# Kernel tuning notes

Hardware: AMD Instinct MI355X
Metric: run time of the kernel (lower is better)

The kernel has to match this reference:

```python
import jax, jax.numpy as jnp
import numpy as np

B, S, D = 2, 2048, 4096
H, KVH, HD = 32, 8, 128
N_REP = H // KVH
ROPE_THETA = 10000.0


def setup_inputs() -> dict:
    key = jax.random.key(0)
    ks = jax.random.split(key, 6)
    x_norm = jax.random.normal(ks[0], (B, S, D), dtype=jnp.float32)
    scale = 0.02
    wq = jax.random.normal(ks[1], (H * HD, D), dtype=jnp.float32) * scale
    wk = jax.random.normal(ks[2], (KVH * HD, D), dtype=jnp.float32) * scale
    wv = jax.random.normal(ks[3], (KVH * HD, D), dtype=jnp.float32) * scale
    wo = jax.random.normal(ks[4], (D, H * HD), dtype=jnp.float32) * scale
    # RoPE tables: freqs_cis[t, j] = exp(i * t * theta^{-2j/HD})
    inv_freq = 1.0 / (ROPE_THETA ** (jnp.arange(0, HD, 2, dtype=jnp.float32) / HD))  # [HD/2]
    angles = jnp.arange(S, dtype=jnp.float32)[:, None] * inv_freq[None, :]  # [S, HD/2]
    freqs_cos = jnp.cos(angles)
    freqs_sin = jnp.sin(angles)
    # causal additive mask (0 on/below diagonal, -1e9 above)
    mask = jnp.where(jnp.arange(S)[None, :] > jnp.arange(S)[:, None], jnp.float32(-1e9), jnp.float32(0.0))
    return {"x_norm": x_norm, "wq": wq, "wk": wk, "wv": wv, "wo": wo,
            "freqs_cos": freqs_cos, "freqs_sin": freqs_sin, "mask": mask, "start_pos": 0}


def _apply_rope(t, cos, sin):
    # t: [B, S, h, HD]; cos/sin: [S, HD/2] -> rotate consecutive pairs
    tr = t.reshape(*t.shape[:-1], HD // 2, 2)
    t0, t1 = tr[..., 0], tr[..., 1]
    c = cos[None, :, None, :]
    s = sin[None, :, None, :]
    out = jnp.stack([t0 * c - t1 * s, t0 * s + t1 * c], axis=-1)
    return out.reshape(t.shape)


def reference(x_norm, wq, wk, wv, wo, freqs_cos, freqs_sin, mask, start_pos):
    # QKV projections (torch Linear: y = x @ W.T)
    xq = jnp.einsum("bsd,ed->bse", x_norm, wq).reshape(B, S, H, HD)
    xk = jnp.einsum("bsd,ed->bse", x_norm, wk).reshape(B, S, KVH, HD)
    xv = jnp.einsum("bsd,ed->bse", x_norm, wv).reshape(B, S, KVH, HD)
    xq = _apply_rope(xq, freqs_cos, freqs_sin)
    xk = _apply_rope(xk, freqs_cos, freqs_sin)
    # start_pos == 0 prefill: cache slice [:start_pos+seqlen] == freshly written xk/xv
    keys = jnp.repeat(xk, N_REP, axis=2)    # [B, S, H, HD] (GQA repeat_kv)
    values = jnp.repeat(xv, N_REP, axis=2)  # [B, S, H, HD]
    scale = 1.0 / np.sqrt(HD).astype(np.float32)
    scores = jnp.einsum("bqhd,bkhd->bhqk", xq, keys) * scale
    scores = scores + mask[None, None, :, :]
    probs = jax.nn.softmax(scores.astype(jnp.float32), axis=-1).astype(xq.dtype)
    out = jnp.einsum("bhqk,bkhd->bqhd", probs, values).reshape(B, S, H * HD)
    return jnp.einsum("bse,de->bsd", out, wo)
```

## Files before the change

kernel.cpp:

```cpp
#include <hip/hip_runtime.h>
#include <stdint.h>

#define B_N 2
#define S_N 2048
#define D_N 4096
#define H_N 32
#define KVH_N 8
#define HD_N 128
#define NQT (S_N / 64)
#define QK_SCALE 0.08838834764831845f

typedef __attribute__((ext_vector_type(8))) short bf16x8;
typedef __attribute__((ext_vector_type(4))) float f32x4;

__device__ __forceinline__ unsigned short f2bf(float f) {
    union { float f; unsigned u; } v; v.f = f;
    unsigned u = v.u;
    u += 0x7fffu + ((u >> 16) & 1u);
    return (unsigned short)(u >> 16);
}
__device__ __forceinline__ float bf2f(unsigned short h) {
    union { unsigned u; float f; } v; v.u = ((unsigned)h) << 16;
    return v.f;
}

__device__ __forceinline__ void gl16(const unsigned short* g, unsigned short* l) {
    __builtin_amdgcn_global_load_lds(
        (const __attribute__((address_space(1))) void*)g,
        (__attribute__((address_space(3))) void*)l, 16, 0, 0);
}

__global__ void __launch_bounds__(256) conv_f32_bf16(const float* __restrict__ in,
                                                     unsigned short* __restrict__ out) {
    int i = (blockIdx.x * 256 + threadIdx.x) * 4;
    float4 v = *(const float4*)(in + i);
    ushort4 o;
    o.x = f2bf(v.x); o.y = f2bf(v.y); o.z = f2bf(v.z); o.w = f2bf(v.w);
    *(ushort4*)(out + i) = o;
}

template<int HEADS, int STRIDE>
__global__ void __launch_bounds__(256) rope_kernel(unsigned short* __restrict__ t,
                                                   const float* __restrict__ cosb,
                                                   const float* __restrict__ sinb,
                                                   float scale) {
    int p = blockIdx.x * 256 + threadIdx.x;
    int i = p & 63;
    int hr = p >> 6;
    int m = hr / HEADS;
    int hh = hr - m * HEADS;
    int s = m & (S_N - 1);
    size_t off = (size_t)m * STRIDE + hh * HD_N + 2 * i;
    unsigned v = *(const unsigned*)(t + off);
    float t0 = bf2f((unsigned short)(v & 0xffffu));
    float t1 = bf2f((unsigned short)(v >> 16));
    float c = cosb[s * 64 + i], sn = sinb[s * 64 + i];
    float o0 = (t0 * c - t1 * sn) * scale;
    float o1 = (t0 * sn + t1 * c) * scale;
    *(unsigned*)(t + off) = (unsigned)f2bf(o0) | ((unsigned)f2bf(o1) << 16);
}


#define BAR() __builtin_amdgcn_s_barrier()
#define VMC4() asm volatile("s_waitcnt vmcnt(4)" ::: "memory")

template<int F32OUT>
__global__ void __launch_bounds__(512, 2)
gemm256(const unsigned short* __restrict__ A, const unsigned short* __restrict__ Bm,
        void* __restrict__ Cv, int M, int N, int K) {
    __shared__ unsigned short ldsA[2][16384];
    __shared__ unsigned short ldsB[2][16384];

    const int tid = threadIdx.x;
    const int lane = tid & 63;
    const int w = tid >> 6;
    const int li = lane & 15, lg = lane >> 4;
    const int wr = w >> 2, wc = w & 3;

    const int nwg = gridDim.x;
    const int cpx = nwg >> 3;
    const int wg = (blockIdx.x & 7) * cpx + (blockIdx.x >> 3);
    const int nbn = N >> 8;
    const int bm = wg / nbn, bn = wg - bm * nbn;
    const int m0 = bm << 8, n0 = bn << 8;

    const int rbase = ((tid >> 7) << 4) + ((tid >> 2) & 15);
    const int cstg = ((tid >> 6) & 1) * 32 + (((tid & 3) * 8) ^ (((tid >> 5) & 1) << 4));
    const unsigned short* Asrc[4];
    const unsigned short* Bsrc[4];
#pragma unroll
    for (int hj = 0; hj < 4; ++hj) {
        Asrc[hj] = A + (size_t)(m0 + hj * 64 + rbase) * K + cstg;
        Bsrc[hj] = Bm + (size_t)(n0 + hj * 64 + rbase) * K + cstg;
    }
    const int dstoff = tid * 8;
    const int kmask = K - 1;

    f32x4 acc[8][4];
#pragma unroll
    for (int i = 0; i < 8; ++i)
#pragma unroll
        for (int j = 0; j < 4; ++j) acc[i][j] = (f32x4){0.f, 0.f, 0.f, 0.f};

    const int colpart = (lg * 16) ^ ((li >> 3) << 5);

#define STG(SRC, LDSBUF, H, T) do {                                         \
        int kk_ = ((T) * 64) & kmask;                                       \
        gl16(SRC[(H)*2 + 0] + kk_, &LDSBUF[((H)*2 + 0) * 4096 + dstoff]);   \
        gl16(SRC[(H)*2 + 1] + kk_, &LDSBUF[((H)*2 + 1) * 4096 + dstoff]);   \
    } while (0)

#define LDB(buf) do {                                                        \
        _Pragma("unroll")                                                    \
        for (int ni_ = 0; ni_ < 4; ++ni_) {                                  \
            _Pragma("unroll")                                                \
            for (int ks_ = 0; ks_ < 2; ++ks_)                                \
                bfr[ni_][ks_] = *(const bf16x8*)((const char*)&ldsB[buf][0]  \
                    + (wc * 4 + ni_) * 2048 + ks_ * 1024 + li * 64 + colpart); \
        }                                                                    \
    } while (0)

#define LDA(buf, q) do {                                                     \
        _Pragma("unroll")                                                    \
        for (int m_ = 0; m_ < 2; ++m_) {                                     \
            _Pragma("unroll")                                                \
            for (int ks_ = 0; ks_ < 2; ++ks_)                                \
                af[m_][ks_] = *(const bf16x8*)((const char*)&ldsA[buf][0]    \
                    + (wr * 8 + (q) * 2 + m_) * 2048 + ks_ * 1024 + li * 64 + colpart); \
        }                                                                    \
    } while (0)

#define MFMAQ(q) do {                                                        \
        __builtin_amdgcn_s_setprio(1);                                       \
        _Pragma("unroll")                                                    \
        for (int ks_ = 0; ks_ < 2; ++ks_) {                                  \
            _Pragma("unroll")                                                \
            for (int m_ = 0; m_ < 2; ++m_) {                                 \
                _Pragma("unroll")                                            \
                for (int ni_ = 0; ni_ < 4; ++ni_)                            \
                    acc[(q)*2 + m_][ni_] = __builtin_amdgcn_mfma_f32_16x16x32_bf16( \
                        af[m_][ks_], bfr[ni_][ks_], acc[(q)*2 + m_][ni_], 0, 0, 0); \
            }                                                                \
        }                                                                    \
        __builtin_amdgcn_s_setprio(0);                                       \
    } while (0)

    STG(Asrc, ldsA[0], 0, 0); STG(Asrc, ldsA[0], 1, 0);
    STG(Bsrc, ldsB[0], 0, 0); STG(Bsrc, ldsB[0], 1, 0);
    STG(Bsrc, ldsB[1], 0, 1); STG(Bsrc, ldsB[1], 1, 1);
    VMC4();
    BAR();

    const int NIT = K >> 7;
    bf16x8 bfr[4][2], af[2][2];
#pragma unroll 1
    for (int i = 0; i < NIT; ++i) {
        const int T = 2 * i;
        LDB(0); LDA(0, 0);
        STG(Asrc, ldsA[1], 0, T + 1);
        BAR(); MFMAQ(0); BAR();
        LDA(0, 1);
        STG(Asrc, ldsA[1], 1, T + 1);
        STG(Bsrc, ldsB[0], 0, T + 2);
        BAR(); MFMAQ(1); BAR();
        LDA(0, 2);
        STG(Bsrc, ldsB[0], 1, T + 2);
        BAR(); MFMAQ(2); BAR();
        LDA(0, 3);
        BAR(); MFMAQ(3); VMC4(); BAR();
        LDB(1); LDA(1, 0);
        STG(Asrc, ldsA[0], 0, T + 2);
        BAR(); MFMAQ(0); BAR();
        LDA(1, 1);
        STG(Asrc, ldsA[0], 1, T + 2);
        BAR(); MFMAQ(1); BAR();
        LDA(1, 2);
        STG(Bsrc, ldsB[1], 0, T + 3);
        BAR(); MFMAQ(2); BAR();
        LDA(1, 3);
        STG(Bsrc, ldsB[1], 1, T + 3);
        BAR(); MFMAQ(3); VMC4(); BAR();
    }

    const int r0 = m0 + wr * 128 + lg * 4;
    const int c0 = n0 + wc * 64 + li;
    if (F32OUT) {
        float* C = (float*)Cv;
#pragma unroll
        for (int mi = 0; mi < 8; ++mi)
#pragma unroll
            for (int ni = 0; ni < 4; ++ni)
#pragma unroll
                for (int rr = 0; rr < 4; ++rr)
                    C[(size_t)(r0 + mi * 16 + rr) * N + c0 + ni * 16] = acc[mi][ni][rr];
    } else {
        unsigned short* C = (unsigned short*)Cv;
#pragma unroll
        for (int mi = 0; mi < 8; ++mi)
#pragma unroll
            for (int ni = 0; ni < 4; ++ni)
#pragma unroll
                for (int rr = 0; rr < 4; ++rr)
                    C[(size_t)(r0 + mi * 16 + rr) * N + c0 + ni * 16] = f2bf(acc[mi][ni][rr]);
    }
#undef STG
#undef LDB
#undef LDA
#undef MFMAQ
}

__device__ __forceinline__ void stage_k_tile(const unsigned short* kt_base,
                                             unsigned short* ks_base, int w, int lane) {
#pragma unroll
    for (int j = 0; j < 2; ++j) {
        int row = (w * 2 + j) * 4 + (lane >> 4);
        int colb = (lane & 15) * 16;
        int key = (row & 7) << 4;
        gl16(kt_base + (size_t)row * 2048 + ((colb ^ key) >> 1),
             ks_base + (w * 2 + j) * 512);
    }
}

__device__ __forceinline__ void load_v(const unsigned short* vt_base, int tid, uint4& a0, uint4& a1) {
    int kv = (tid >> 4) * 2, d0 = (tid & 15) * 8;
    const unsigned short* vp = vt_base + (size_t)kv * 2048 + d0;
    a0 = *(const uint4*)vp;
    a1 = *(const uint4*)(vp + 2048);
}

__device__ __forceinline__ void write_v(unsigned short* vt_lds, int tid, uint4 a0, uint4 a1) {
    int kv = (tid >> 4) * 2, d0 = (tid & 15) * 8;
    union { uint4 q; unsigned short u[8]; } x0, x1;
    x0.q = a0; x1.q = a1;
#pragma unroll
    for (int jj = 0; jj < 8; ++jj) {
        int d = d0 + jj;
        unsigned pack = (unsigned)x0.u[jj] | ((unsigned)x1.u[jj] << 16);
        int key = ((d ^ (d >> 3)) & 7) << 4;
        *(unsigned*)((char*)vt_lds + d * 128 + ((kv * 2) ^ key)) = pack;
    }
}

__global__ void __launch_bounds__(512) attn_kernel(const unsigned short* __restrict__ Q,
                                                   const unsigned short* __restrict__ Kb,
                                                   const unsigned short* __restrict__ Vb,
                                                   unsigned short* __restrict__ O) {
    __shared__ unsigned short Ks[2][64 * 128];
    __shared__ unsigned short Vt[2][128 * 64];
    __shared__ unsigned short Ps[8][32 * 64];

    const int pidx = blockIdx.x;
    const int bg = blockIdx.y;
    const int b = bg >> 3, kvh = bg & 7;
    const int tid = threadIdx.x;
    const int w = tid >> 6, lane = tid & 63;
    const int li = lane & 15, lg = lane >> 4;
    const int h = kvh * 4 + (w >> 1);
    const int qh = (w & 1) * 32;

    unsigned short* Pw = &Ps[w][0];
    const unsigned short* KVrow0 = Kb + (size_t)b * S_N * 2048 + kvh * 128;
    const unsigned short* Vrow0  = Vb + (size_t)b * S_N * 2048 + kvh * 128;

#pragma unroll 1
    for (int pass = 0; pass < 2; ++pass) {
        const int qt = pass ? (NQT - 1 - pidx) : pidx;
        const int nt = qt + 1;

        bf16x8 qf[2][4];
        {
            const unsigned short* qp = Q + ((size_t)b * S_N + qt * 64 + qh + li) * (H_N * HD_N)
                                         + h * HD_N + lg * 8;
#pragma unroll
            for (int mi = 0; mi < 2; ++mi)
#pragma unroll
                for (int ds = 0; ds < 4; ++ds)
                    qf[mi][ds] = *(const bf16x8*)(qp + (size_t)mi * 16 * (H_N * HD_N) + ds * 32);
        }

        float mreg[2][4], lreg[2][4];
#pragma unroll
        for (int mi = 0; mi < 2; ++mi)
#pragma unroll
            for (int r = 0; r < 4; ++r) { mreg[mi][r] = -1e30f; lreg[mi][r] = 0.f; }
        f32x4 o_acc[2][8];
#pragma unroll
        for (int mi = 0; mi < 2; ++mi)
#pragma unroll
            for (int di = 0; di < 8; ++di) o_acc[mi][di] = (f32x4){0.f, 0.f, 0.f, 0.f};

        {
            stage_k_tile(KVrow0, &Ks[0][0], w, lane);
            uint4 a0, a1;
            load_v(Vrow0, tid, a0, a1);
            write_v(&Vt[0][0], tid, a0, a1);
        }
        __syncthreads();

#pragma unroll 1
        for (int t = 0; t < nt; ++t) {
            const int c = t & 1;
            const bool pre = (t + 1 < nt);
            uint4 a0, a1;
            if (pre) {
                stage_k_tile(KVrow0 + (size_t)(t + 1) * 64 * 2048, &Ks[c ^ 1][0], w, lane);
                load_v(Vrow0 + (size_t)(t + 1) * 64 * 2048, tid, a0, a1);
            }

            f32x4 sf[2][4];
#pragma unroll
            for (int mi = 0; mi < 2; ++mi)
#pragma unroll
                for (int ni = 0; ni < 4; ++ni) sf[mi][ni] = (f32x4){0.f, 0.f, 0.f, 0.f};
#pragma unroll
            for (int ni = 0; ni < 4; ++ni) {
                const int kvc = ni * 16 + li;
                const int kkey = (kvc & 7) << 4;
                bf16x8 kf[4];
#pragma unroll
                for (int ds = 0; ds < 4; ++ds)
                    kf[ds] = *(const bf16x8*)((char*)&Ks[c][0] + kvc * 256
                                              + ((ds * 64 + lg * 16) ^ kkey));
#pragma unroll
                for (int mi = 0; mi < 2; ++mi)
#pragma unroll
                    for (int ds = 0; ds < 4; ++ds)
                        sf[mi][ni] = __builtin_amdgcn_mfma_f32_16x16x32_bf16(qf[mi][ds], kf[ds], sf[mi][ni], 0, 0, 0);
            }

            if (t == qt) {
#pragma unroll
                for (int mi = 0; mi < 2; ++mi)
#pragma unroll
                    for (int ni = 0; ni < 4; ++ni) {
                        int kvc = ni * 16 + li;
#pragma unroll
                        for (int r = 0; r < 4; ++r) {
                            int qg = qh + mi * 16 + lg * 4 + r;
                            if (kvc > qg) sf[mi][ni][r] = -1e30f;
                        }
                    }
            }

            float fac[2][4];
#pragma unroll
            for (int mi = 0; mi < 2; ++mi)
#pragma unroll
                for (int r = 0; r < 4; ++r) {
                    float pm = fmaxf(fmaxf(sf[mi][0][r], sf[mi][1][r]), fmaxf(sf[mi][2][r], sf[mi][3][r]));
                    pm = fmaxf(pm, __shfl_xor(pm, 1));
                    pm = fmaxf(pm, __shfl_xor(pm, 2));
                    pm = fmaxf(pm, __shfl_xor(pm, 4));
                    pm = fmaxf(pm, __shfl_xor(pm, 8));
                    float mn = fmaxf(mreg[mi][r], pm);
                    fac[mi][r] = __expf(mreg[mi][r] - mn);
                    mreg[mi][r] = mn;
                }
#pragma unroll
            for (int mi = 0; mi < 2; ++mi)
#pragma unroll
                for (int ni = 0; ni < 4; ++ni)
#pragma unroll
                    for (int r = 0; r < 4; ++r)
                        sf[mi][ni][r] = __expf(sf[mi][ni][r] - mreg[mi][r]);
#pragma unroll
            for (int mi = 0; mi < 2; ++mi)
#pragma unroll
                for (int r = 0; r < 4; ++r) {
                    float s = sf[mi][0][r] + sf[mi][1][r] + sf[mi][2][r] + sf[mi][3][r];
                    s += __shfl_xor(s, 1);
                    s += __shfl_xor(s, 2);
                    s += __shfl_xor(s, 4);
                    s += __shfl_xor(s, 8);
                    lreg[mi][r] = lreg[mi][r] * fac[mi][r] + s;
                }
#pragma unroll
            for (int mi = 0; mi < 2; ++mi)
#pragma unroll
                for (int di = 0; di < 8; ++di)
#pragma unroll
                    for (int r = 0; r < 4; ++r) o_acc[mi][di][r] *= fac[mi][r];

#pragma unroll
            for (int mi = 0; mi < 2; ++mi)
#pragma unroll
                for (int ni = 0; ni < 4; ++ni) {
#pragma unroll
                    for (int r = 0; r < 4; ++r) {
                        int q = mi * 16 + lg * 4 + r;
                        int kv = ni * 16 + li;
                        *(unsigned short*)((char*)Pw + q * 128 + ((kv * 2) ^ ((q & 7) << 4)))
                            = f2bf(sf[mi][ni][r]);
                    }
                }

            {
                bf16x8 pf[2][2];
#pragma unroll
                for (int mi = 0; mi < 2; ++mi) {
                    int q = mi * 16 + li;
                    int pkey = (q & 7) << 4;
#pragma unroll
                    for (int ks = 0; ks < 2; ++ks)
                        pf[mi][ks] = *(const bf16x8*)((char*)Pw + q * 128
                                                      + ((ks * 64 + lg * 16) ^ pkey));
                }
#pragma unroll
                for (int di = 0; di < 8; ++di) {
                    int d = di * 16 + li;
                    int vkey = ((d ^ (d >> 3)) & 7) << 4;
                    bf16x8 vf[2];
#pragma unroll
                    for (int ks = 0; ks < 2; ++ks)
                        vf[ks] = *(const bf16x8*)((char*)&Vt[c][0] + d * 128
                                                  + ((ks * 64 + lg * 16) ^ vkey));
#pragma unroll
                    for (int mi = 0; mi < 2; ++mi)
#pragma unroll
                        for (int ks = 0; ks < 2; ++ks)
                            o_acc[mi][di] = __builtin_amdgcn_mfma_f32_16x16x32_bf16(pf[mi][ks], vf[ks], o_acc[mi][di], 0, 0, 0);
                }
            }

            if (pre) write_v(&Vt[c ^ 1][0], tid, a0, a1);
            __syncthreads();
        }

        float inv[2][4];
#pragma unroll
        for (int mi = 0; mi < 2; ++mi)
#pragma unroll
            for (int r = 0; r < 4; ++r) inv[mi][r] = 1.f / lreg[mi][r];
        unsigned short* op = O + ((size_t)b * S_N + qt * 64 + qh + lg * 4) * (H_N * HD_N)
                               + h * HD_N + li;
#pragma unroll
        for (int mi = 0; mi < 2; ++mi)
#pragma unroll
            for (int di = 0; di < 8; ++di)
#pragma unroll
                for (int r = 0; r < 4; ++r)
                    op[((size_t)(mi * 16 + r)) * (H_N * HD_N) + di * 16]
                        = f2bf(o_acc[mi][di][r] * inv[mi][r]);
    }
}

extern "C" void kernel_launch(void* const* d_in, const int* in_sizes, int n_in,
                              void* d_out, int out_size, void* d_ws, size_t ws_size,
                              hipStream_t stream) {
    (void)in_sizes; (void)n_in; (void)out_size; (void)ws_size;
    const float* x  = (const float*)d_in[0];
    const float* wq = (const float*)d_in[1];
    const float* wk = (const float*)d_in[2];
    const float* wv = (const float*)d_in[3];
    const float* wo = (const float*)d_in[4];
    const float* fc = (const float*)d_in[5];
    const float* fs = (const float*)d_in[6];
    float* out = (float*)d_out;

    char* ws = (char*)d_ws;
    unsigned short* xb  = (unsigned short*)(ws);
    unsigned short* wb  = (unsigned short*)(ws + 33554432);
    unsigned short* wkv = (unsigned short*)(ws + 67108864);
    unsigned short* Qb  = (unsigned short*)(ws + 83886080);
    unsigned short* KVb = (unsigned short*)(ws + 117440512);

    const int BS = B_N * S_N;

    conv_f32_bf16<<<dim3(BS * D_N / 1024), 256, 0, stream>>>(x, xb);
    conv_f32_bf16<<<dim3(H_N * HD_N * D_N / 1024), 256, 0, stream>>>(wq, wb);
    conv_f32_bf16<<<dim3(KVH_N * HD_N * D_N / 1024), 256, 0, stream>>>(wk, wkv);
    conv_f32_bf16<<<dim3(KVH_N * HD_N * D_N / 1024), 256, 0, stream>>>(wv, wkv + KVH_N * HD_N * D_N);

    gemm256<0><<<dim3((BS / 256) * (D_N / 256)), 512, 0, stream>>>(xb, wb, Qb, BS, D_N, D_N);
    conv_f32_bf16<<<dim3(D_N * H_N * HD_N / 1024), 256, 0, stream>>>(wo, wb);
    gemm256<0><<<dim3((BS / 256) * (2048 / 256)), 512, 0, stream>>>(xb, wkv, KVb, BS, 2048, D_N);

    rope_kernel<H_N, H_N * HD_N><<<dim3(BS * H_N * 64 / 256), 256, 0, stream>>>(Qb, fc, fs, QK_SCALE);
    rope_kernel<KVH_N, 2 * KVH_N * HD_N><<<dim3(BS * KVH_N * 64 / 256), 256, 0, stream>>>(KVb, fc, fs, 1.0f);

    attn_kernel<<<dim3(NQT / 2, B_N * KVH_N), 512, 0, stream>>>(Qb, KVb, KVb + 1024, Qb);

    gemm256<1><<<dim3((BS / 256) * (D_N / 256)), 512, 0, stream>>>(Qb, wb, out, BS, D_N, D_N);
}
```

Measured before the change: 637.2 us.

## Keep softmax probabilities in registers via transposed QK^T and split heads per block

The attention kernel now computes S^T (K as the A operand) so each lane holds one query row's scores. The probabilities can then be packed straight into bf16 MFMA operands with v_cvt_pk_bf16, which removes the per-wave LDS round trip for P and its buffer. Softmax uses exp2 with log2(e) folded into the Q scale applied in RoPE. Row reductions use two cross-lane shuffles, and the rescale factors are broadcast back with shuffles. Blocks shrink to 256 threads handling two heads each with launch_bounds(256,2), doubling the grid; each K/V tile is now loaded once per two heads instead of once per four.

```diff
diff --git a/kernel.cpp b/kernel.cpp
--- a/kernel.cpp
+++ b/kernel.cpp
@@ -8,7 +8,7 @@
 #define KVH_N 8
 #define HD_N 128
 #define NQT (S_N / 64)
-#define QK_SCALE 0.08838834764831845f
+#define QS_LOG2E 0.12751743f
 
 typedef __attribute__((ext_vector_type(8))) short bf16x8;
 typedef __attribute__((ext_vector_type(4))) float f32x4;
@@ -22,6 +22,11 @@
 __device__ __forceinline__ float bf2f(unsigned short h) {
     union { unsigned u; float f; } v; v.u = ((unsigned)h) << 16;
     return v.f;
+}
+__device__ __forceinline__ unsigned cvt_pk_bf16(float lo, float hi) {
+    unsigned r;
+    asm("v_cvt_pk_bf16_f32 %0, %1, %2" : "=v"(r) : "v"(lo), "v"(hi));
+    return r;
 }
 
 __device__ __forceinline__ void gl16(const unsigned short* g, unsigned short* l) {
@@ -59,7 +64,6 @@
     float o1 = (t0 * sn + t1 * c) * scale;
     *(unsigned*)(t + off) = (unsigned)f2bf(o0) | ((unsigned)f2bf(o1) << 16);
 }
-
 
 #define BAR() __builtin_amdgcn_s_barrier()
 #define VMC4() asm volatile("s_waitcnt vmcnt(4)" ::: "memory")
@@ -209,56 +213,63 @@
 #undef MFMAQ
 }
 
-__device__ __forceinline__ void stage_k_tile(const unsigned short* kt_base,
-                                             unsigned short* ks_base, int w, int lane) {
-#pragma unroll
-    for (int j = 0; j < 2; ++j) {
-        int row = (w * 2 + j) * 4 + (lane >> 4);
+
+__device__ __forceinline__ void stage_k_tile4(const unsigned short* kt_base,
+                                              unsigned short* ks_base, int w, int lane) {
+#pragma unroll
+    for (int j = 0; j < 4; ++j) {
+        int row = (w * 4 + j) * 4 + (lane >> 4);
         int colb = (lane & 15) * 16;
         int key = (row & 7) << 4;
         gl16(kt_base + (size_t)row * 2048 + ((colb ^ key) >> 1),
-             ks_base + (w * 2 + j) * 512);
-    }
-}
-
-__device__ __forceinline__ void load_v(const unsigned short* vt_base, int tid, uint4& a0, uint4& a1) {
-    int kv = (tid >> 4) * 2, d0 = (tid & 15) * 8;
-    const unsigned short* vp = vt_base + (size_t)kv * 2048 + d0;
-    a0 = *(const uint4*)vp;
-    a1 = *(const uint4*)(vp + 2048);
-}
-
-__device__ __forceinline__ void write_v(unsigned short* vt_lds, int tid, uint4 a0, uint4 a1) {
-    int kv = (tid >> 4) * 2, d0 = (tid & 15) * 8;
-    union { uint4 q; unsigned short u[8]; } x0, x1;
-    x0.q = a0; x1.q = a1;
-#pragma unroll
-    for (int jj = 0; jj < 8; ++jj) {
-        int d = d0 + jj;
-        unsigned pack = (unsigned)x0.u[jj] | ((unsigned)x1.u[jj] << 16);
-        int key = ((d ^ (d >> 3)) & 7) << 4;
-        *(unsigned*)((char*)vt_lds + d * 128 + ((kv * 2) ^ key)) = pack;
-    }
-}
-
-__global__ void __launch_bounds__(512) attn_kernel(const unsigned short* __restrict__ Q,
-                                                   const unsigned short* __restrict__ Kb,
-                                                   const unsigned short* __restrict__ Vb,
-                                                   unsigned short* __restrict__ O) {
+             ks_base + (w * 4 + j) * 512);
+    }
+}
+
+__device__ __forceinline__ void load_v2(const unsigned short* vt_base, int tid, uint4 a[2][2]) {
+#pragma unroll
+    for (int it = 0; it < 2; ++it) {
+        int c = it * 256 + tid;
+        int kv = (c >> 4) * 2, d0 = (c & 15) * 8;
+        const unsigned short* vp = vt_base + (size_t)kv * 2048 + d0;
+        a[it][0] = *(const uint4*)vp;
+        a[it][1] = *(const uint4*)(vp + 2048);
+    }
+}
+
+__device__ __forceinline__ void write_v2(unsigned short* vt_lds, int tid, uint4 a[2][2]) {
+#pragma unroll
+    for (int it = 0; it < 2; ++it) {
+        int c = it * 256 + tid;
+        int kv = (c >> 4) * 2, d0 = (c & 15) * 8;
+        union { uint4 q; unsigned short u[8]; } x0, x1;
+        x0.q = a[it][0]; x1.q = a[it][1];
+#pragma unroll
+        for (int jj = 0; jj < 8; ++jj) {
+            int d = d0 + jj;
+            unsigned pack = (unsigned)x0.u[jj] | ((unsigned)x1.u[jj] << 16);
+            int key = ((d ^ (d >> 3)) & 7) << 4;
+            *(unsigned*)((char*)vt_lds + d * 128 + ((kv * 2) ^ key)) = pack;
+        }
+    }
+}
+
+__global__ void __launch_bounds__(256, 2) attn_kernel(const unsigned short* __restrict__ Q,
+                                                      const unsigned short* __restrict__ Kb,
+                                                      const unsigned short* __restrict__ Vb,
+                                                      unsigned short* __restrict__ O) {
     __shared__ unsigned short Ks[2][64 * 128];
     __shared__ unsigned short Vt[2][128 * 64];
-    __shared__ unsigned short Ps[8][32 * 64];
 
     const int pidx = blockIdx.x;
     const int bg = blockIdx.y;
-    const int b = bg >> 3, kvh = bg & 7;
+    const int b = bg >> 4, kvh = (bg >> 1) & 7, hp = bg & 1;
     const int tid = threadIdx.x;
     const int w = tid >> 6, lane = tid & 63;
     const int li = lane & 15, lg = lane >> 4;
-    const int h = kvh * 4 + (w >> 1);
+    const int h = kvh * 4 + hp * 2 + (w >> 1);
     const int qh = (w & 1) * 32;
 
-    unsigned short* Pw = &Ps[w][0];
     const unsigned short* KVrow0 = Kb + (size_t)b * S_N * 2048 + kvh * 128;
     const unsigned short* Vrow0  = Vb + (size_t)b * S_N * 2048 + kvh * 128;
 
@@ -278,22 +289,20 @@
                     qf[mi][ds] = *(const bf16x8*)(qp + (size_t)mi * 16 * (H_N * HD_N) + ds * 32);
         }
 
-        float mreg[2][4], lreg[2][4];
+        float mreg[2], lreg[2];
+#pragma unroll
+        for (int mi = 0; mi < 2; ++mi) { mreg[mi] = -1e30f; lreg[mi] = 0.f; }
+        f32x4 o_acc[2][8];
 #pragma unroll
         for (int mi = 0; mi < 2; ++mi)
 #pragma unroll
-            for (int r = 0; r < 4; ++r) { mreg[mi][r] = -1e30f; lreg[mi][r] = 0.f; }
-        f32x4 o_acc[2][8];
-#pragma unroll
-        for (int mi = 0; mi < 2; ++mi)
-#pragma unroll
             for (int di = 0; di < 8; ++di) o_acc[mi][di] = (f32x4){0.f, 0.f, 0.f, 0.f};
 
         {
-            stage_k_tile(KVrow0, &Ks[0][0], w, lane);
-            uint4 a0, a1;
-            load_v(Vrow0, tid, a0, a1);
-            write_v(&Vt[0][0], tid, a0, a1);
+            stage_k_tile4(KVrow0, &Ks[0][0], w, lane);
+            uint4 a[2][2];
+            load_v2(Vrow0, tid, a);
+            write_v2(&Vt[0][0], tid, a);
         }
         __syncthreads();
 
@@ -301,17 +310,17 @@
         for (int t = 0; t < nt; ++t) {
             const int c = t & 1;
             const bool pre = (t + 1 < nt);
-            uint4 a0, a1;
+            uint4 a[2][2];
             if (pre) {
-                stage_k_tile(KVrow0 + (size_t)(t + 1) * 64 * 2048, &Ks[c ^ 1][0], w, lane);
-                load_v(Vrow0 + (size_t)(t + 1) * 64 * 2048, tid, a0, a1);
+                stage_k_tile4(KVrow0 + (size_t)(t + 1) * 64 * 2048, &Ks[c ^ 1][0], w, lane);
+                load_v2(Vrow0 + (size_t)(t + 1) * 64 * 2048, tid, a);
             }
 
-            f32x4 sf[2][4];
+            f32x4 sT[2][4];
 #pragma unroll
             for (int mi = 0; mi < 2; ++mi)
 #pragma unroll
-                for (int ni = 0; ni < 4; ++ni) sf[mi][ni] = (f32x4){0.f, 0.f, 0.f, 0.f};
+                for (int ni = 0; ni < 4; ++ni) sT[mi][ni] = (f32x4){0.f, 0.f, 0.f, 0.f};
 #pragma unroll
             for (int ni = 0; ni < 4; ++ni) {
                 const int kvc = ni * 16 + li;
@@ -325,122 +334,115 @@
                 for (int mi = 0; mi < 2; ++mi)
 #pragma unroll
                     for (int ds = 0; ds < 4; ++ds)
-                        sf[mi][ni] = __builtin_amdgcn_mfma_f32_16x16x32_bf16(qf[mi][ds], kf[ds], sf[mi][ni], 0, 0, 0);
+                        sT[mi][ni] = __builtin_amdgcn_mfma_f32_16x16x32_bf16(kf[ds], qf[mi][ds], sT[mi][ni], 0, 0, 0);
             }
 
             if (t == qt) {
 #pragma unroll
-                for (int mi = 0; mi < 2; ++mi)
-#pragma unroll
-                    for (int ni = 0; ni < 4; ++ni) {
-                        int kvc = ni * 16 + li;
-#pragma unroll
-                        for (int r = 0; r < 4; ++r) {
-                            int qg = qh + mi * 16 + lg * 4 + r;
-                            if (kvc > qg) sf[mi][ni][r] = -1e30f;
-                        }
-                    }
-            }
-
-            float fac[2][4];
-#pragma unroll
-            for (int mi = 0; mi < 2; ++mi)
-#pragma unroll
-                for (int r = 0; r < 4; ++r) {
-                    float pm = fmaxf(fmaxf(sf[mi][0][r], sf[mi][1][r]), fmaxf(sf[mi][2][r], sf[mi][3][r]));
-                    pm = fmaxf(pm, __shfl_xor(pm, 1));
-                    pm = fmaxf(pm, __shfl_xor(pm, 2));
-                    pm = fmaxf(pm, __shfl_xor(pm, 4));
-                    pm = fmaxf(pm, __shfl_xor(pm, 8));
-                    float mn = fmaxf(mreg[mi][r], pm);
-                    fac[mi][r] = __expf(mreg[mi][r] - mn);
-                    mreg[mi][r] = mn;
-                }
-#pragma unroll
-            for (int mi = 0; mi < 2; ++mi)
-#pragma unroll
-                for (int ni = 0; ni < 4; ++ni)
-#pragma unroll
-                    for (int r = 0; r < 4; ++r)
-                        sf[mi][ni][r] = __expf(sf[mi][ni][r] - mreg[mi][r]);
-#pragma unroll
-            for (int mi = 0; mi < 2; ++mi)
-#pragma unroll
-                for (int r = 0; r < 4; ++r) {
-                    float s = sf[mi][0][r] + sf[mi][1][r] + sf[mi][2][r] + sf[mi][3][r];
-                    s += __shfl_xor(s, 1);
-                    s += __shfl_xor(s, 2);
-                    s += __shfl_xor(s, 4);
-                    s += __shfl_xor(s, 8);
-                    lreg[mi][r] = lreg[mi][r] * fac[mi][r] + s;
-                }
-#pragma unroll
-            for (int mi = 0; mi < 2; ++mi)
-#pragma unroll
-                for (int di = 0; di < 8; ++di)
-#pragma unroll
-                    for (int r = 0; r < 4; ++r) o_acc[mi][di][r] *= fac[mi][r];
-
-#pragma unroll
-            for (int mi = 0; mi < 2; ++mi)
-#pragma unroll
-                for (int ni = 0; ni < 4; ++ni) {
-#pragma unroll
-                    for (int r = 0; r < 4; ++r) {
-                        int q = mi * 16 + lg * 4 + r;
-                        int kv = ni * 16 + li;
-                        *(unsigned short*)((char*)Pw + q * 128 + ((kv * 2) ^ ((q & 7) << 4)))
-                            = f2bf(sf[mi][ni][r]);
-                    }
-                }
-
-            {
-                bf16x8 pf[2][2];
-#pragma unroll
                 for (int mi = 0; mi < 2; ++mi) {
-                    int q = mi * 16 + li;
-                    int pkey = (q & 7) << 4;
-#pragma unroll
-                    for (int ks = 0; ks < 2; ++ks)
-                        pf[mi][ks] = *(const bf16x8*)((char*)Pw + q * 128
-                                                      + ((ks * 64 + lg * 16) ^ pkey));
-                }
-#pragma unroll
-                for (int di = 0; di < 8; ++di) {
-                    int d = di * 16 + li;
-                    int vkey = ((d ^ (d >> 3)) & 7) << 4;
-                    bf16x8 vf[2];
-#pragma unroll
-                    for (int ks = 0; ks < 2; ++ks)
-                        vf[ks] = *(const bf16x8*)((char*)&Vt[c][0] + d * 128
-                                                  + ((ks * 64 + lg * 16) ^ vkey));
-#pragma unroll
-                    for (int mi = 0; mi < 2; ++mi)
-#pragma unroll
-                        for (int ks = 0; ks < 2; ++ks)
-                            o_acc[mi][di] = __builtin_amdgcn_mfma_f32_16x16x32_bf16(pf[mi][ks], vf[ks], o_acc[mi][di], 0, 0, 0);
+                    int qq = qh + mi * 16 + li;
+#pragma unroll
+                    for (int ni = 0; ni < 4; ++ni)
+#pragma unroll
+                        for (int r = 0; r < 4; ++r)
+                            if (ni * 16 + lg * 4 + r > qq) sT[mi][ni][r] = -1e30f;
                 }
             }
 
-            if (pre) write_v(&Vt[c ^ 1][0], tid, a0, a1);
+            float fac0[2];
+#pragma unroll
+            for (int mi = 0; mi < 2; ++mi) {
+                float pm = sT[mi][0][0];
+#pragma unroll
+                for (int ni = 0; ni < 4; ++ni)
+#pragma unroll
+                    for (int r = 0; r < 4; ++r) pm = fmaxf(pm, sT[mi][ni][r]);
+                pm = fmaxf(pm, __shfl_xor(pm, 16));
+                pm = fmaxf(pm, __shfl_xor(pm, 32));
+                float mn = fmaxf(mreg[mi], pm);
+                fac0[mi] = __builtin_amdgcn_exp2f(mreg[mi] - mn);
+                mreg[mi] = mn;
+#pragma unroll
+                for (int ni = 0; ni < 4; ++ni)
+#pragma unroll
+                    for (int r = 0; r < 4; ++r)
+                        sT[mi][ni][r] = __builtin_amdgcn_exp2f(sT[mi][ni][r] - mn);
+                float rs = 0.f;
+#pragma unroll
+                for (int ni = 0; ni < 4; ++ni)
+#pragma unroll
+                    for (int r = 0; r < 4; ++r) rs += sT[mi][ni][r];
+                rs += __shfl_xor(rs, 16);
+                rs += __shfl_xor(rs, 32);
+                lreg[mi] = lreg[mi] * fac0[mi] + rs;
+            }
+
+            float facR[2][4];
+#pragma unroll
+            for (int mi = 0; mi < 2; ++mi)
+#pragma unroll
+                for (int rr = 0; rr < 4; ++rr)
+                    facR[mi][rr] = __shfl(fac0[mi], (lg << 4) | (lg * 4 + rr));
+#pragma unroll
+            for (int mi = 0; mi < 2; ++mi)
+#pragma unroll
+                for (int di = 0; di < 8; ++di)
+#pragma unroll
+                    for (int rr = 0; rr < 4; ++rr) o_acc[mi][di][rr] *= facR[mi][rr];
+
+            union U { bf16x8 v; unsigned u[4]; };
+            U pa[2][2];
+#pragma unroll
+            for (int mi = 0; mi < 2; ++mi)
+#pragma unroll
+                for (int ks = 0; ks < 2; ++ks) {
+                    pa[mi][ks].u[0] = cvt_pk_bf16(sT[mi][2 * ks][0], sT[mi][2 * ks][1]);
+                    pa[mi][ks].u[1] = cvt_pk_bf16(sT[mi][2 * ks][2], sT[mi][2 * ks][3]);
+                    pa[mi][ks].u[2] = cvt_pk_bf16(sT[mi][2 * ks + 1][0], sT[mi][2 * ks + 1][1]);
+                    pa[mi][ks].u[3] = cvt_pk_bf16(sT[mi][2 * ks + 1][2], sT[mi][2 * ks + 1][3]);
+                }
+
+#pragma unroll
+            for (int di = 0; di < 8; ++di) {
+                int d = di * 16 + li;
+                int vkey = ((d ^ (d >> 3)) & 7) << 4;
+                const char* vbase = (const char*)&Vt[c][0] + d * 128;
+                bf16x8 vf[2];
+#pragma unroll
+                for (int ks = 0; ks < 2; ++ks) {
+                    union { bf16x8 v; unsigned long long g[2]; } vv;
+                    int cb = ks * 64 + lg * 8;
+                    vv.g[0] = *(const unsigned long long*)(vbase + (cb ^ vkey));
+                    vv.g[1] = *(const unsigned long long*)(vbase + ((cb + 32) ^ vkey));
+                    vf[ks] = vv.v;
+                }
+#pragma unroll
+                for (int mi = 0; mi < 2; ++mi)
+#pragma unroll
+                    for (int ks = 0; ks < 2; ++ks)
+                        o_acc[mi][di] = __builtin_amdgcn_mfma_f32_16x16x32_bf16(pa[mi][ks].v, vf[ks], o_acc[mi][di], 0, 0, 0);
+            }
+
+            if (pre) write_v2(&Vt[c ^ 1][0], tid, a);
             __syncthreads();
         }
 
-        float inv[2][4];
-#pragma unroll
-        for (int mi = 0; mi < 2; ++mi)
-#pragma unroll
-            for (int r = 0; r < 4; ++r) inv[mi][r] = 1.f / lreg[mi][r];
         unsigned short* op = O + ((size_t)b * S_N + qt * 64 + qh + lg * 4) * (H_N * HD_N)
                                + h * HD_N + li;
 #pragma unroll
-        for (int mi = 0; mi < 2; ++mi)
+        for (int mi = 0; mi < 2; ++mi) {
+            float iv = 1.f / lreg[mi];
+            float ivR[4];
+#pragma unroll
+            for (int rr = 0; rr < 4; ++rr)
+                ivR[rr] = __shfl(iv, (lg << 4) | (lg * 4 + rr));
 #pragma unroll
             for (int di = 0; di < 8; ++di)
 #pragma unroll
-                for (int r = 0; r < 4; ++r)
-                    op[((size_t)(mi * 16 + r)) * (H_N * HD_N) + di * 16]
-                        = f2bf(o_acc[mi][di][r] * inv[mi][r]);
+                for (int rr = 0; rr < 4; ++rr)
+                    op[((size_t)(mi * 16 + rr)) * (H_N * HD_N) + di * 16]
+                        = f2bf(o_acc[mi][di][rr] * ivR[rr]);
+        }
     }
 }
 
@@ -475,10 +477,10 @@
     conv_f32_bf16<<<dim3(D_N * H_N * HD_N / 1024), 256, 0, stream>>>(wo, wb);
     gemm256<0><<<dim3((BS / 256) * (2048 / 256)), 512, 0, stream>>>(xb, wkv, KVb, BS, 2048, D_N);
 
-    rope_kernel<H_N, H_N * HD_N><<<dim3(BS * H_N * 64 / 256), 256, 0, stream>>>(Qb, fc, fs, QK_SCALE);
+    rope_kernel<H_N, H_N * HD_N><<<dim3(BS * H_N * 64 / 256), 256, 0, stream>>>(Qb, fc, fs, QS_LOG2E);
     rope_kernel<KVH_N, 2 * KVH_N * HD_N><<<dim3(BS * KVH_N * 64 / 256), 256, 0, stream>>>(KVb, fc, fs, 1.0f);
 
-    attn_kernel<<<dim3(NQT / 2, B_N * KVH_N), 512, 0, stream>>>(Qb, KVb, KVb + 1024, Qb);
+    attn_kernel<<<dim3(NQT / 2, B_N * KVH_N * 2), 256, 0, stream>>>(Qb, KVb, KVb + 1024, Qb);
 
     gemm256<1><<<dim3((BS / 256) * (D_N / 256)), 512, 0, stream>>>(Qb, wb, out, BS, D_N, D_N);
 }
```

Result: slower. 656.2 us (+3.0%).
